# Kernel optimization log

Hardware: AMD Instinct MI355X
Metric: run time of the kernel (lower is better)

Reference implementation:

```python
import jax, jax.numpy as jnp
import numpy as np

TEMP = 0.1
QUEUE_SIZE = 512
CUTOFF_KM = 25.0
EARTH_R_KM = 6371.0088


def _normalize(x, eps=1e-12):
    # F.normalize: x / max(||x||, eps)
    n = jnp.linalg.norm(x, axis=-1, keepdims=True)
    return x / jnp.maximum(n, eps)


def _haversine_km(g1, g2):
    # g1: (B,2) [lat,lon] degrees; g2: (S,2) -> (B,S) great-circle km
    r = jnp.pi / 180.0
    lat1 = g1[:, 0:1] * r
    lon1 = g1[:, 1:2] * r
    lat2 = g2[None, :, 0] * r
    lon2 = g2[None, :, 1] * r
    dlat = lat2 - lat1
    dlon = lon2 - lon1
    a = jnp.sin(dlat / 2) ** 2 + jnp.cos(lat1) * jnp.cos(lat2) * jnp.sin(dlon / 2) ** 2
    return 2.0 * EARTH_R_KM * jnp.arcsin(jnp.sqrt(jnp.clip(a, 0.0, 1.0)))


def setup_inputs() -> dict:
    key = jax.random.key(0)
    k = jax.random.split(key, 7)
    n_aug, B, D, S = 4, 256, 768, 65536
    V = jax.random.normal(k[0], (n_aug, B, D), jnp.float32)
    L = jax.random.normal(k[1], (B, D), jnp.float32)
    gps = jnp.concatenate([
        jax.random.uniform(k[2], (B, 1), jnp.float32, -90.0, 90.0),
        jax.random.uniform(k[3], (B, 1), jnp.float32, -180.0, 180.0)], axis=1)
    support_features = jax.random.normal(k[4], (S, D), jnp.float32)
    support_gps = jnp.concatenate([
        jax.random.uniform(k[5], (S, 1), jnp.float32, -90.0, 90.0),
        jax.random.uniform(k[6], (S, 1), jnp.float32, -180.0, 180.0)], axis=1)
    return {"V": V, "L": L, "gps": gps,
            "support_features": support_features, "support_gps": support_gps}


def reference(V, L, gps, support_features, support_gps):
    # org joint embedding always from V[0]; nearest neighbour over raw support feats
    org = _normalize(V[0] * L)                                   # (B,D)
    sim = org @ support_features.T                               # (B,S)
    nn_idx = jnp.argmax(sim, axis=1)                             # (B,)
    nn = _normalize(support_features[nn_idx])                    # (B,D)

    # augmented joints for j = 1..n_aug-1
    augs = _normalize(V[1:] * L[None])                           # (J,B,D)
    # numerator always uses V[1] (as in the original code), constant over j
    num = jnp.einsum('bd,bd->b', nn, augs[0]) / TEMP             # (B,)

    # in-batch denominator: sum_i exp(nn_b . aug_{j,i} / T)
    batch_den = jnp.exp(jnp.einsum('bd,jid->jbi', nn, augs) / TEMP).sum(axis=2)  # (J,B)

    # GPS-filtered negative queue: first QUEUE_SIZE support entries > 25 km away,
    # zero-padded (zero rows contribute exp(0) = 1, matching the torch code)
    mask = _haversine_km(gps, support_gps) > CUTOFF_KM           # (B,S)
    order = jnp.argsort(jnp.where(mask, 0, 1), axis=1)[:, :QUEUE_SIZE]  # stable: kept in original order
    valid = jnp.take_along_axis(mask, order, axis=1)             # (B,Q)
    qfeat = support_features[order] * valid[..., None]           # (B,Q,D)
    queue_den = jnp.exp(jnp.einsum('bd,bqd->bq', nn, qfeat) / TEMP).sum(axis=1)  # (B,)

    den = jnp.log(batch_den + queue_den[None, :])                # (J,B)
    loss = -(num[None, :] - den).sum() / V.shape[1]
    return loss
```

## Files before the change

kernel.cpp:

```cpp
#include <hip/hip_runtime.h>
#include <hip/hip_bf16.h>

#define B_ROWS 256
#define S_SUP  65536
#define D_DIM  768
#define QSZ    512
#define NCH    12
#define ABYTES 32768
#define BBYTES 16384

typedef short bf16x8 __attribute__((ext_vector_type(8)));
typedef float f32x4  __attribute__((ext_vector_type(4)));
typedef float f32x16 __attribute__((ext_vector_type(16)));

__device__ __forceinline__ bf16x8 cvt8(float4 a, float4 b) {
  bf16x8 r;
  r[0] = (short)(__float_as_uint(a.x) >> 16);
  r[1] = (short)(__float_as_uint(a.y) >> 16);
  r[2] = (short)(__float_as_uint(a.z) >> 16);
  r[3] = (short)(__float_as_uint(a.w) >> 16);
  r[4] = (short)(__float_as_uint(b.x) >> 16);
  r[5] = (short)(__float_as_uint(b.y) >> 16);
  r[6] = (short)(__float_as_uint(b.z) >> 16);
  r[7] = (short)(__float_as_uint(b.w) >> 16);
  return r;
}

__device__ __forceinline__ void gl_lds16(const void* g, void* l) {
  __builtin_amdgcn_global_load_lds(
      (const __attribute__((address_space(1))) unsigned int*)g,
      (__attribute__((address_space(3))) unsigned int*)l, 16, 0, 0);
}

__device__ __forceinline__ float block_sum(float v) {
  __shared__ float tmp[4];
  #pragma unroll
  for (int m = 32; m >= 1; m >>= 1) v += __shfl_xor(v, m, 64);
  __syncthreads();
  if ((threadIdx.x & 63) == 0) tmp[threadIdx.x >> 6] = v;
  __syncthreads();
  return tmp[0] + tmp[1] + tmp[2] + tmp[3];
}

__device__ __forceinline__ double block_sum_d(double v) {
  __shared__ double tmp[4];
  #pragma unroll
  for (int m = 32; m >= 1; m >>= 1) v += __shfl_xor(v, m, 64);
  __syncthreads();
  if ((threadIdx.x & 63) == 0) tmp[threadIdx.x >> 6] = v;
  __syncthreads();
  return tmp[0] + tmp[1] + tmp[2] + tmp[3];
}

__global__ __launch_bounds__(256) void init_kernel(unsigned long long* gmax, double* bden) {
  int t = threadIdx.x;
  gmax[t] = 0ull;
  for (int i = t; i < 3 * B_ROWS; i += 256) bden[i] = 0.0;
}

__global__ __launch_bounds__(256) void prep_kernel(const float* __restrict__ V,
                                                   const float* __restrict__ L,
                                                   unsigned short* __restrict__ orgb,
                                                   float* __restrict__ augs) {
  int jb = blockIdx.x;
  int j = jb >> 8, b = jb & 255;
  int tid = threadIdx.x;
  __shared__ float srow[D_DIM];
  const float* v = V + ((size_t)j * B_ROWS + b) * D_DIM;
  const float* l = L + (size_t)b * D_DIM;
  float p[3]; float ssq = 0.f;
  #pragma unroll
  for (int i = 0; i < 3; ++i) {
    int k = tid + 256 * i;
    p[i] = v[k] * l[k];
    ssq += p[i] * p[i];
  }
  ssq = block_sum(ssq);
  float inv = 1.0f / fmaxf(sqrtf(ssq), 1e-12f);
  if (j == 0) {
    #pragma unroll
    for (int i = 0; i < 3; ++i) srow[tid + 256 * i] = p[i] * inv;
    __syncthreads();
    if (tid < 96) {
      int k0 = tid * 8;
      float4 f0 = *(const float4*)&srow[k0];
      float4 f1 = *(const float4*)&srow[k0 + 4];
      bf16x8 hv = cvt8(f0, f1);
      int c = k0 >> 6, g = (k0 >> 3) & 7;
      *(bf16x8*)(orgb + c * 16384 + g * 2048 + b * 8) = hv;
    }
  } else {
    float* dst = augs + ((size_t)(j - 1) * B_ROWS + b) * D_DIM;
    #pragma unroll
    for (int i = 0; i < 3; ++i) dst[tid + 256 * i] = p[i] * inv;
  }
}

__global__ __launch_bounds__(512, 4) void sim_argmax_kernel(const unsigned short* __restrict__ orgb,
                                                            const float* __restrict__ sf,
                                                            unsigned long long* __restrict__ gmax) {
  const int tid = threadIdx.x;
  const int w   = tid >> 6;
  const int l   = tid & 63;
  const int h   = l >> 5;
  const int c31 = l & 31;
  const int wr  = w >> 1;
  const int wc  = w & 1;
  const int s0  = blockIdx.x * 128;

  __shared__ __align__(16) char smem[ABYTES + BBYTES];

  f32x16 acc[4];
  #pragma unroll
  for (int t = 0; t < 4; ++t)
    #pragma unroll
    for (int r = 0; r < 16; ++r) acc[t][r] = 0.f;

  const int bs = tid >> 2;
  const int ko = (tid & 3) * 16;
  const float* bsrc0 = sf + (size_t)(s0 + bs) * D_DIM + ko;
  const int g0 = ko >> 3;
  char* bw0 = smem + ABYTES + g0 * 2048 + ((bs ^ g0) & 127) * 16;
  char* bw1 = smem + ABYTES + (g0 + 1) * 2048 + ((bs ^ (g0 + 1)) & 127) * 16;

  const char* agbase = (const char*)orgb + w * 1024 + l * 16;
  char* aldst0 = smem + 0 * 8192 + w * 1024;
  char* aldst1 = smem + 1 * 8192 + w * 1024;
  char* aldst2 = smem + 2 * 8192 + w * 1024;
  char* aldst3 = smem + 3 * 8192 + w * 1024;

  const int ar0 = wr * 64 + c31;
  const int ar1 = ar0 + 32;
  const int bs0 = wc * 64 + c31;
  const int bs1 = bs0 + 32;

  for (int c = 0; c < NCH; ++c) {
    const float4* bp = (const float4*)(bsrc0 + c * 64);
    float4 f0 = bp[0], f1 = bp[1], f2 = bp[2], f3 = bp[3];
    {
      const char* g = agbase + c * ABYTES;
      gl_lds16(g,         aldst0);
      gl_lds16(g +  8192, aldst1);
      gl_lds16(g + 16384, aldst2);
      gl_lds16(g + 24576, aldst3);
    }
    *(bf16x8*)bw0 = cvt8(f0, f1);
    *(bf16x8*)bw1 = cvt8(f2, f3);
    __syncthreads();

    #pragma unroll
    for (int ks = 0; ks < 4; ++ks) {
      int g = ks * 2 + h;
      bf16x8 a0 = *(const bf16x8*)(smem + g * 4096 + ar0 * 16);
      bf16x8 a1 = *(const bf16x8*)(smem + g * 4096 + ar1 * 16);
      bf16x8 b0 = *(const bf16x8*)(smem + ABYTES + g * 2048 + ((bs0 ^ g) & 127) * 16);
      bf16x8 b1 = *(const bf16x8*)(smem + ABYTES + g * 2048 + ((bs1 ^ g) & 127) * 16);
      acc[0] = __builtin_amdgcn_mfma_f32_32x32x16_bf16(a0, b0, acc[0], 0, 0, 0);
      acc[1] = __builtin_amdgcn_mfma_f32_32x32x16_bf16(a0, b1, acc[1], 0, 0, 0);
      acc[2] = __builtin_amdgcn_mfma_f32_32x32x16_bf16(a1, b0, acc[2], 0, 0, 0);
      acc[3] = __builtin_amdgcn_mfma_f32_32x32x16_bf16(a1, b1, acc[3], 0, 0, 0);
    }
    __syncthreads();
  }

  float* smax = (float*)smem;
  int*   sidx = (int*)(smem + 2048);
  #pragma unroll
  for (int t = 0; t < 2; ++t) {
    #pragma unroll
    for (int rg = 0; rg < 16; ++rg) {
      float v0 = acc[t * 2 + 0][rg];
      float v1 = acc[t * 2 + 1][rg];
      int i0 = s0 + wc * 64 + c31;
      int i1 = i0 + 32;
      float v; int idx;
      if (v1 > v0) { v = v1; idx = i1; } else { v = v0; idx = i0; }
      #pragma unroll
      for (int m = 1; m < 32; m <<= 1) {
        float ov = __shfl_xor(v, m, 64);
        int   oi = __shfl_xor(idx, m, 64);
        if (ov > v || (ov == v && oi < idx)) { v = ov; idx = oi; }
      }
      if (c31 == 0) {
        int row = wr * 64 + t * 32 + (rg & 3) + 8 * (rg >> 2) + 4 * h;
        smax[wc * 256 + row] = v;
        sidx[wc * 256 + row] = idx;
      }
    }
  }
  __syncthreads();
  if (tid < 256) {
    int b = tid;
    float v  = smax[b];       int idx = sidx[b];
    float ov = smax[256 + b]; int oi  = sidx[256 + b];
    if (ov > v || (ov == v && oi < idx)) { v = ov; idx = oi; }
    unsigned u = __float_as_uint(v);
    unsigned key = (u & 0x80000000u) ? ~u : (u | 0x80000000u);
    unsigned long long packed = ((unsigned long long)key << 32) |
                                (unsigned long long)(0xFFFFFFFFu - (unsigned)idx);
    if (packed > gmax[b]) atomicMax(gmax + b, packed);
  }
}

__global__ __launch_bounds__(256) void nn_kernel(const unsigned long long* __restrict__ gmax,
                                                 const float* __restrict__ sf,
                                                 const float* __restrict__ augs,
                                                 float* __restrict__ nn,
                                                 float* __restrict__ nnT,
                                                 float* __restrict__ num) {
  int b = blockIdx.x, tid = threadIdx.x;
  int idx = (int)(0xFFFFFFFFu - (unsigned)(gmax[b] & 0xFFFFFFFFull));
  const float* row = sf + (size_t)idx * D_DIM;
  float p[3]; float ssq = 0.f;
  #pragma unroll
  for (int i = 0; i < 3; ++i) { p[i] = row[tid + 256 * i]; ssq += p[i] * p[i]; }
  ssq = block_sum(ssq);
  float inv = 1.0f / fmaxf(sqrtf(ssq), 1e-12f);
  const float* a0 = augs + (size_t)b * D_DIM;
  float dot = 0.f;
  #pragma unroll
  for (int i = 0; i < 3; ++i) {
    int k = tid + 256 * i;
    float nv = p[i] * inv;
    nn[(size_t)b * D_DIM + k] = nv;
    nnT[(size_t)k * B_ROWS + b] = nv;
    dot += nv * a0[k];
  }
  dot = block_sum(dot);
  if (tid == 0) num[b] = dot * 10.0f;
}

__global__ __launch_bounds__(256) void bden_kernel(const float* __restrict__ augs,
                                                   const float* __restrict__ nnT,
                                                   double* __restrict__ bden) {
  int jc = blockIdx.x;
  int j = jc >> 6, c = jc & 63;
  int i0 = c * 4;
  __shared__ float s_aug[4 * D_DIM];
  const float* src = augs + ((size_t)j * B_ROWS + i0) * D_DIM;
  for (int idx = threadIdx.x; idx < 4 * D_DIM; idx += 256) s_aug[idx] = src[idx];
  __syncthreads();
  int b = threadIdx.x;
  float a0 = 0.f, a1 = 0.f, a2 = 0.f, a3 = 0.f;
  for (int k = 0; k < D_DIM; ++k) {
    float nv = nnT[(size_t)k * B_ROWS + b];
    a0 += nv * s_aug[k];
    a1 += nv * s_aug[D_DIM + k];
    a2 += nv * s_aug[2 * D_DIM + k];
    a3 += nv * s_aug[3 * D_DIM + k];
  }
  double v = exp((double)a0 * 10.0) + exp((double)a1 * 10.0) +
             exp((double)a2 * 10.0) + exp((double)a3 * 10.0);
  atomicAdd(&bden[j * B_ROWS + b], v);
}

__global__ __launch_bounds__(256) void queue_kernel(const float* __restrict__ gps,
                                                    const float* __restrict__ sgps,
                                                    const float* __restrict__ sf,
                                                    const float* __restrict__ nn,
                                                    double* __restrict__ qden) {
  int b = blockIdx.x, tid = threadIdx.x;
  int w = tid >> 6, lane = tid & 63;
  __shared__ int qidx[QSZ];
  __shared__ int s_count;
  __shared__ int s_wcnt[4];
  __shared__ __align__(16) float s_nn[D_DIM];
  __shared__ double s_gsum[16];
  for (int k = tid; k < D_DIM; k += 256) s_nn[k] = nn[(size_t)b * D_DIM + k];
  if (tid == 0) s_count = 0;
  __syncthreads();

  const float r = 0.017453292519943295f;
  float lat1 = gps[b * 2 + 0] * r, lon1 = gps[b * 2 + 1] * r;
  float cl1 = cosf(lat1);
  int base = 0;
  while (true) {
    int count = s_count;
    if (count >= QSZ || base >= S_SUP) break;
    int s = base + tid;
    float lat2 = sgps[s * 2 + 0] * r, lon2 = sgps[s * 2 + 1] * r;
    float sdlat = sinf((lat2 - lat1) * 0.5f);
    float sdlon = sinf((lon2 - lon1) * 0.5f);
    float a = sdlat * sdlat + cl1 * cosf(lat2) * sdlon * sdlon;
    a = fminf(fmaxf(a, 0.f), 1.f);
    float d = 2.0f * 6371.0088f * asinf(sqrtf(a));
    bool valid = d > 25.0f;

    unsigned long long m = __ballot(valid);
    int wcnt = __popcll(m);
    if (lane == 0) s_wcnt[w] = wcnt;
    __syncthreads();
    int wbase = count;
    for (int i = 0; i < w; ++i) wbase += s_wcnt[i];
    int pos = wbase + __popcll(m & ((1ull << lane) - 1ull));
    if (valid && pos < QSZ) qidx[pos] = s;
    __syncthreads();
    if (tid == 0) {
      int total = s_wcnt[0] + s_wcnt[1] + s_wcnt[2] + s_wcnt[3];
      s_count = min(QSZ, count + total);
    }
    base += 256;
    __syncthreads();
  }
  int count = s_count;

  int g  = lane >> 4;
  int l2 = lane & 15;
  double acc = 0.0;
  const float4* nn4 = (const float4*)s_nn;
  for (int q = w * 4 + g; q < count; q += 16) {
    const float4* row = (const float4*)(sf + (size_t)qidx[q] * D_DIM);
    float dot = 0.f;
    #pragma unroll
    for (int i = 0; i < 12; ++i) {
      float4 a = row[l2 + 16 * i];
      float4 nv = nn4[l2 + 16 * i];
      dot += a.x * nv.x + a.y * nv.y + a.z * nv.z + a.w * nv.w;
    }
    #pragma unroll
    for (int m2 = 8; m2 >= 1; m2 >>= 1) dot += __shfl_xor(dot, m2, 16);
    if (l2 == 0) acc += exp((double)dot * 10.0);
  }
  if (l2 == 0) s_gsum[w * 4 + g] = acc;
  __syncthreads();
  if (tid == 0) {
    double t = (double)(QSZ - count);
    #pragma unroll
    for (int i = 0; i < 16; ++i) t += s_gsum[i];
    qden[b] = t;
  }
}

__global__ __launch_bounds__(256) void loss_kernel(const float* __restrict__ num,
                                                   const double* __restrict__ bden,
                                                   const double* __restrict__ qden,
                                                   float* __restrict__ out) {
  int b = threadIdx.x;
  double q = qden[b];
  double n = (double)num[b];
  double t = 0.0;
  #pragma unroll
  for (int j = 0; j < 3; ++j) t += n - log(bden[j * B_ROWS + b] + q);
  t = block_sum_d(t);
  if (b == 0) out[0] = (float)(-t / 256.0);
}

extern "C" void kernel_launch(void* const* d_in, const int* in_sizes, int n_in,
                              void* d_out, int out_size, void* d_ws, size_t ws_size,
                              hipStream_t stream) {
  const float* V    = (const float*)d_in[0];
  const float* L    = (const float*)d_in[1];
  const float* gps  = (const float*)d_in[2];
  const float* sf   = (const float*)d_in[3];
  const float* sgps = (const float*)d_in[4];
  float* out = (float*)d_out;

  char* ws = (char*)d_ws;
  size_t off = 0;
  unsigned short* orgb = (unsigned short*)(ws + off); off += 393216;
  float* augs = (float*)(ws + off); off += 2359296;
  float* nn   = (float*)(ws + off); off += 786432;
  float* nnT  = (float*)(ws + off); off += 786432;
  float* num  = (float*)(ws + off); off += 1024;
  double* bden = (double*)(ws + off); off += 6144;
  double* qden = (double*)(ws + off); off += 2048;
  unsigned long long* gmax = (unsigned long long*)(ws + off); off += 2048;

  init_kernel<<<1, 256, 0, stream>>>(gmax, bden);
  prep_kernel<<<1024, 256, 0, stream>>>(V, L, orgb, augs);
  sim_argmax_kernel<<<S_SUP / 128, 512, 0, stream>>>(orgb, sf, gmax);
  nn_kernel<<<B_ROWS, 256, 0, stream>>>(gmax, sf, augs, nn, nnT, num);
  bden_kernel<<<192, 256, 0, stream>>>(augs, nnT, bden);
  queue_kernel<<<B_ROWS, 256, 0, stream>>>(gps, sgps, sf, nn, qden);
  loss_kernel<<<1, 256, 0, stream>>>(num, bden, qden, out);
}
```

Measured before the change: 394.4 us.

## Restructure sim GEMM: per-wave support rows direct from global, larger A chunks

The similarity/argmax kernel now has each wave own 32 support rows, loading and converting them straight from global memory into MFMA B operands with register prefetch, instead of staging them through LDS. A 256-column K-chunk of the bf16 query matrix (128 KB) goes into LDS, giving 3 chunk iterations instead of 12. Each block covers 256 support rows and reduces the argmax across 8 waves. This cuts LDS traffic for B and the number of barriers, but uses more accumulator registers and more LDS, which lowers occupancy to 2 blocks per CU and exposes direct global loads to latency.

```diff
diff --git a/kernel.cpp b/kernel.cpp
--- a/kernel.cpp
+++ b/kernel.cpp
@@ -5,9 +5,9 @@
 #define S_SUP  65536
 #define D_DIM  768
 #define QSZ    512
-#define NCH    12
-#define ABYTES 32768
-#define BBYTES 16384
+#define NCH    3
+#define CHUNK_K 256
+#define ACH_BYTES 131072
 
 typedef short bf16x8 __attribute__((ext_vector_type(8)));
 typedef float f32x4  __attribute__((ext_vector_type(4)));
@@ -86,8 +86,8 @@
       float4 f0 = *(const float4*)&srow[k0];
       float4 f1 = *(const float4*)&srow[k0 + 4];
       bf16x8 hv = cvt8(f0, f1);
-      int c = k0 >> 6, g = (k0 >> 3) & 7;
-      *(bf16x8*)(orgb + c * 16384 + g * 2048 + b * 8) = hv;
+      int c = k0 >> 8, g = (k0 >> 3) & 31;
+      *(bf16x8*)(orgb + c * 65536 + g * 2048 + b * 8) = hv;
     }
   } else {
     float* dst = augs + ((size_t)(j - 1) * B_ROWS + b) * D_DIM;
@@ -96,7 +96,7 @@
   }
 }
 
-__global__ __launch_bounds__(512, 4) void sim_argmax_kernel(const unsigned short* __restrict__ orgb,
+__global__ __launch_bounds__(512, 2) void sim_argmax_kernel(const unsigned short* __restrict__ orgb,
                                                             const float* __restrict__ sf,
                                                             unsigned long long* __restrict__ gmax) {
   const int tid = threadIdx.x;
@@ -104,77 +104,59 @@
   const int l   = tid & 63;
   const int h   = l >> 5;
   const int c31 = l & 31;
-  const int wr  = w >> 1;
-  const int wc  = w & 1;
-  const int s0  = blockIdx.x * 128;
-
-  __shared__ __align__(16) char smem[ABYTES + BBYTES];
-
-  f32x16 acc[4];
-  #pragma unroll
-  for (int t = 0; t < 4; ++t)
-    #pragma unroll
-    for (int r = 0; r < 16; ++r) acc[t][r] = 0.f;
-
-  const int bs = tid >> 2;
-  const int ko = (tid & 3) * 16;
-  const float* bsrc0 = sf + (size_t)(s0 + bs) * D_DIM + ko;
-  const int g0 = ko >> 3;
-  char* bw0 = smem + ABYTES + g0 * 2048 + ((bs ^ g0) & 127) * 16;
-  char* bw1 = smem + ABYTES + (g0 + 1) * 2048 + ((bs ^ (g0 + 1)) & 127) * 16;
-
-  const char* agbase = (const char*)orgb + w * 1024 + l * 16;
-  char* aldst0 = smem + 0 * 8192 + w * 1024;
-  char* aldst1 = smem + 1 * 8192 + w * 1024;
-  char* aldst2 = smem + 2 * 8192 + w * 1024;
-  char* aldst3 = smem + 3 * 8192 + w * 1024;
-
-  const int ar0 = wr * 64 + c31;
-  const int ar1 = ar0 + 32;
-  const int bs0 = wc * 64 + c31;
-  const int bs1 = bs0 + 32;
+  const int s0  = blockIdx.x * 256;
+  const int myrow = s0 + w * 32 + c31;
+
+  __shared__ __align__(16) char smem[ACH_BYTES];
+
+  f32x16 accs[8];
+  #pragma unroll
+  for (int t = 0; t < 8; ++t)
+    #pragma unroll
+    for (int r = 0; r < 16; ++r) accs[t][r] = 0.f;
+
+  const char* sfb = (const char*)sf + (size_t)myrow * 3072 + h * 32;
+  const char* agbase = (const char*)orgb + tid * 16;
+  char* adst = smem + tid * 16;
 
   for (int c = 0; c < NCH; ++c) {
-    const float4* bp = (const float4*)(bsrc0 + c * 64);
-    float4 f0 = bp[0], f1 = bp[1], f2 = bp[2], f3 = bp[3];
     {
-      const char* g = agbase + c * ABYTES;
-      gl_lds16(g,         aldst0);
-      gl_lds16(g +  8192, aldst1);
-      gl_lds16(g + 16384, aldst2);
-      gl_lds16(g + 24576, aldst3);
-    }
-    *(bf16x8*)bw0 = cvt8(f0, f1);
-    *(bf16x8*)bw1 = cvt8(f2, f3);
-    __syncthreads();
-
-    #pragma unroll
-    for (int ks = 0; ks < 4; ++ks) {
-      int g = ks * 2 + h;
-      bf16x8 a0 = *(const bf16x8*)(smem + g * 4096 + ar0 * 16);
-      bf16x8 a1 = *(const bf16x8*)(smem + g * 4096 + ar1 * 16);
-      bf16x8 b0 = *(const bf16x8*)(smem + ABYTES + g * 2048 + ((bs0 ^ g) & 127) * 16);
-      bf16x8 b1 = *(const bf16x8*)(smem + ABYTES + g * 2048 + ((bs1 ^ g) & 127) * 16);
-      acc[0] = __builtin_amdgcn_mfma_f32_32x32x16_bf16(a0, b0, acc[0], 0, 0, 0);
-      acc[1] = __builtin_amdgcn_mfma_f32_32x32x16_bf16(a0, b1, acc[1], 0, 0, 0);
-      acc[2] = __builtin_amdgcn_mfma_f32_32x32x16_bf16(a1, b0, acc[2], 0, 0, 0);
-      acc[3] = __builtin_amdgcn_mfma_f32_32x32x16_bf16(a1, b1, acc[3], 0, 0, 0);
+      const char* g = agbase + c * ACH_BYTES;
+      #pragma unroll
+      for (int i = 0; i < 16; ++i)
+        gl_lds16(g + i * 8192, adst + i * 8192);
+    }
+    __syncthreads();
+
+    const char* brow = sfb + c * 1024;
+    float4 nb0 = *(const float4*)(brow);
+    float4 nb1 = *(const float4*)(brow + 16);
+    #pragma unroll
+    for (int ks = 0; ks < 16; ++ks) {
+      float4 cb0 = nb0, cb1 = nb1;
+      if (ks < 15) {
+        nb0 = *(const float4*)(brow + (ks + 1) * 64);
+        nb1 = *(const float4*)(brow + (ks + 1) * 64 + 16);
+      }
+      bf16x8 bf = cvt8(cb0, cb1);
+      const char* ab = smem + (ks * 2 + h) * 4096 + c31 * 16;
+      #pragma unroll
+      for (int rt = 0; rt < 8; ++rt) {
+        bf16x8 af = *(const bf16x8*)(ab + rt * 512);
+        accs[rt] = __builtin_amdgcn_mfma_f32_32x32x16_bf16(af, bf, accs[rt], 0, 0, 0);
+      }
     }
     __syncthreads();
   }
 
   float* smax = (float*)smem;
-  int*   sidx = (int*)(smem + 2048);
-  #pragma unroll
-  for (int t = 0; t < 2; ++t) {
+  int*   sidx = (int*)(smem + 8192);
+  #pragma unroll
+  for (int rt = 0; rt < 8; ++rt) {
     #pragma unroll
     for (int rg = 0; rg < 16; ++rg) {
-      float v0 = acc[t * 2 + 0][rg];
-      float v1 = acc[t * 2 + 1][rg];
-      int i0 = s0 + wc * 64 + c31;
-      int i1 = i0 + 32;
-      float v; int idx;
-      if (v1 > v0) { v = v1; idx = i1; } else { v = v0; idx = i0; }
+      float v = accs[rt][rg];
+      int idx = myrow;
       #pragma unroll
       for (int m = 1; m < 32; m <<= 1) {
         float ov = __shfl_xor(v, m, 64);
@@ -182,23 +164,26 @@
         if (ov > v || (ov == v && oi < idx)) { v = ov; idx = oi; }
       }
       if (c31 == 0) {
-        int row = wr * 64 + t * 32 + (rg & 3) + 8 * (rg >> 2) + 4 * h;
-        smax[wc * 256 + row] = v;
-        sidx[wc * 256 + row] = idx;
+        int row = rt * 32 + (rg & 3) + 8 * (rg >> 2) + 4 * h;
+        smax[w * 256 + row] = v;
+        sidx[w * 256 + row] = idx;
       }
     }
   }
   __syncthreads();
   if (tid < 256) {
-    int b = tid;
-    float v  = smax[b];       int idx = sidx[b];
-    float ov = smax[256 + b]; int oi  = sidx[256 + b];
-    if (ov > v || (ov == v && oi < idx)) { v = ov; idx = oi; }
+    int row = tid;
+    float v = smax[row]; int idx = sidx[row];
+    #pragma unroll
+    for (int w2 = 1; w2 < 8; ++w2) {
+      float ov = smax[w2 * 256 + row]; int oi = sidx[w2 * 256 + row];
+      if (ov > v || (ov == v && oi < idx)) { v = ov; idx = oi; }
+    }
     unsigned u = __float_as_uint(v);
     unsigned key = (u & 0x80000000u) ? ~u : (u | 0x80000000u);
     unsigned long long packed = ((unsigned long long)key << 32) |
                                 (unsigned long long)(0xFFFFFFFFu - (unsigned)idx);
-    if (packed > gmax[b]) atomicMax(gmax + b, packed);
+    if (packed > gmax[row]) atomicMax(gmax + row, packed);
   }
 }
 
@@ -368,7 +353,7 @@
 
   init_kernel<<<1, 256, 0, stream>>>(gmax, bden);
   prep_kernel<<<1024, 256, 0, stream>>>(V, L, orgb, augs);
-  sim_argmax_kernel<<<S_SUP / 128, 512, 0, stream>>>(orgb, sf, gmax);
+  sim_argmax_kernel<<<S_SUP / 256, 512, 0, stream>>>(orgb, sf, gmax);
   nn_kernel<<<B_ROWS, 256, 0, stream>>>(gmax, sf, augs, nn, nnT, num);
   bden_kernel<<<192, 256, 0, stream>>>(augs, nnT, bden);
   queue_kernel<<<B_ROWS, 256, 0, stream>>>(gps, sgps, sf, nn, qden);
```

New measurement: 440.8 us. +11.8%, slower.

## Double-buffer LDS tiles in sim-argmax GEMM with register prefetch

Applied to the files above, without the earlier changes.

Restructures the main similarity-argmax GEMM loop so that global loads for the next K-tile go into registers while MFMAs run on the current LDS buffer, then get stored into the alternate buffer. This uses one barrier per iteration instead of two and drops the global_load_lds direct path. LDS grows to 96 KB and launch bounds fall from 4 to 2 blocks per CU, which reduces occupancy and latency hiding across blocks.

```diff
diff --git a/kernel.cpp b/kernel.cpp
--- a/kernel.cpp
+++ b/kernel.cpp
@@ -5,9 +5,10 @@
 #define S_SUP  65536
 #define D_DIM  768
 #define QSZ    512
-#define NCH    12
-#define ABYTES 32768
-#define BBYTES 16384
+#define NKT    12
+#define ASTEP  32768
+#define BSTEP  16384
+#define BBASE  65536
 
 typedef short bf16x8 __attribute__((ext_vector_type(8)));
 typedef float f32x4  __attribute__((ext_vector_type(4)));
@@ -26,12 +27,6 @@
   return r;
 }
 
-__device__ __forceinline__ void gl_lds16(const void* g, void* l) {
-  __builtin_amdgcn_global_load_lds(
-      (const __attribute__((address_space(1))) unsigned int*)g,
-      (__attribute__((address_space(3))) unsigned int*)l, 16, 0, 0);
-}
-
 __device__ __forceinline__ float block_sum(float v) {
   __shared__ float tmp[4];
   #pragma unroll
@@ -96,7 +91,7 @@
   }
 }
 
-__global__ __launch_bounds__(512, 4) void sim_argmax_kernel(const unsigned short* __restrict__ orgb,
+__global__ __launch_bounds__(512, 2) void sim_argmax_kernel(const unsigned short* __restrict__ orgb,
                                                             const float* __restrict__ sf,
                                                             unsigned long long* __restrict__ gmax) {
   const int tid = threadIdx.x;
@@ -108,7 +103,7 @@
   const int wc  = w & 1;
   const int s0  = blockIdx.x * 128;
 
-  __shared__ __align__(16) char smem[ABYTES + BBYTES];
+  __shared__ __align__(16) char smem[98304];
 
   f32x16 acc[4];
   #pragma unroll
@@ -116,62 +111,94 @@
     #pragma unroll
     for (int r = 0; r < 16; ++r) acc[t][r] = 0.f;
 
-  const int bs = tid >> 2;
-  const int ko = (tid & 3) * 16;
-  const float* bsrc0 = sf + (size_t)(s0 + bs) * D_DIM + ko;
-  const int g0 = ko >> 3;
-  char* bw0 = smem + ABYTES + g0 * 2048 + ((bs ^ g0) & 127) * 16;
-  char* bw1 = smem + ABYTES + (g0 + 1) * 2048 + ((bs ^ (g0 + 1)) & 127) * 16;
-
-  const char* agbase = (const char*)orgb + w * 1024 + l * 16;
-  char* aldst0 = smem + 0 * 8192 + w * 1024;
-  char* aldst1 = smem + 1 * 8192 + w * 1024;
-  char* aldst2 = smem + 2 * 8192 + w * 1024;
-  char* aldst3 = smem + 3 * 8192 + w * 1024;
-
-  const int ar0 = wr * 64 + c31;
-  const int ar1 = ar0 + 32;
-  const int bs0 = wc * 64 + c31;
-  const int bs1 = bs0 + 32;
-
-  for (int c = 0; c < NCH; ++c) {
-    const float4* bp = (const float4*)(bsrc0 + c * 64);
-    float4 f0 = bp[0], f1 = bp[1], f2 = bp[2], f3 = bp[3];
-    {
-      const char* g = agbase + c * ABYTES;
-      gl_lds16(g,         aldst0);
-      gl_lds16(g +  8192, aldst1);
-      gl_lds16(g + 16384, aldst2);
-      gl_lds16(g + 24576, aldst3);
-    }
-    *(bf16x8*)bw0 = cvt8(f0, f1);
-    *(bf16x8*)bw1 = cvt8(f2, f3);
-    __syncthreads();
-
+  const char* agbase = (const char*)orgb + tid * 16;
+  const int bsr = tid >> 2;
+  const int bq  = tid & 3;
+  const float* bgbase = sf + (size_t)(s0 + bsr) * D_DIM + bq * 16;
+  const int bg0 = bq * 2;
+  char* bdst0 = smem + BBASE + bg0 * 2048 + (((bsr ^ bg0) & 127) << 4);
+  char* bdst1 = smem + BBASE + (bg0 + 1) * 2048 + (((bsr ^ (bg0 + 1)) & 127) << 4);
+
+  const int arow0 = (wr * 64 + c31) * 16;
+  const int bcol0 = wc * 64 + c31;
+
+  bf16x8 av0, av1, av2, av3;
+  float4 f0, f1, f2, f3;
+
+  {
+    const char* ag = agbase;
+    av0 = *(const bf16x8*)(ag);
+    av1 = *(const bf16x8*)(ag + 8192);
+    av2 = *(const bf16x8*)(ag + 16384);
+    av3 = *(const bf16x8*)(ag + 24576);
+    const float4* bp = (const float4*)bgbase;
+    f0 = bp[0]; f1 = bp[1]; f2 = bp[2]; f3 = bp[3];
+    char* ad = smem + tid * 16;
+    *(bf16x8*)(ad)         = av0;
+    *(bf16x8*)(ad + 8192)  = av1;
+    *(bf16x8*)(ad + 16384) = av2;
+    *(bf16x8*)(ad + 24576) = av3;
+    *(bf16x8*)bdst0 = cvt8(f0, f1);
+    *(bf16x8*)bdst1 = cvt8(f2, f3);
+  }
+  asm volatile("s_waitcnt lgkmcnt(0)" ::: "memory");
+  __builtin_amdgcn_s_barrier();
+  __builtin_amdgcn_sched_barrier(0);
+
+  for (int kt = 0; kt < NKT; ++kt) {
+    const int cur = kt & 1;
+    if (kt < NKT - 1) {
+      const char* ag = agbase + (kt + 1) * ASTEP;
+      av0 = *(const bf16x8*)(ag);
+      av1 = *(const bf16x8*)(ag + 8192);
+      av2 = *(const bf16x8*)(ag + 16384);
+      av3 = *(const bf16x8*)(ag + 24576);
+      const float4* bp = (const float4*)(bgbase + (size_t)(kt + 1) * 64);
+      f0 = bp[0]; f1 = bp[1]; f2 = bp[2]; f3 = bp[3];
+    }
+    __builtin_amdgcn_sched_barrier(0);
+
+    const char* abuf = smem + cur * ASTEP;
+    const char* bbuf = smem + BBASE + cur * BSTEP;
     #pragma unroll
     for (int ks = 0; ks < 4; ++ks) {
-      int g = ks * 2 + h;
-      bf16x8 a0 = *(const bf16x8*)(smem + g * 4096 + ar0 * 16);
-      bf16x8 a1 = *(const bf16x8*)(smem + g * 4096 + ar1 * 16);
-      bf16x8 b0 = *(const bf16x8*)(smem + ABYTES + g * 2048 + ((bs0 ^ g) & 127) * 16);
-      bf16x8 b1 = *(const bf16x8*)(smem + ABYTES + g * 2048 + ((bs1 ^ g) & 127) * 16);
+      const int g = ks * 2 + h;
+      bf16x8 a0 = *(const bf16x8*)(abuf + g * 4096 + arow0);
+      bf16x8 a1 = *(const bf16x8*)(abuf + g * 4096 + arow0 + 512);
+      bf16x8 b0 = *(const bf16x8*)(bbuf + g * 2048 + (((bcol0      ) ^ g) & 127) * 16);
+      bf16x8 b1 = *(const bf16x8*)(bbuf + g * 2048 + (((bcol0 + 32 ) ^ g) & 127) * 16);
       acc[0] = __builtin_amdgcn_mfma_f32_32x32x16_bf16(a0, b0, acc[0], 0, 0, 0);
       acc[1] = __builtin_amdgcn_mfma_f32_32x32x16_bf16(a0, b1, acc[1], 0, 0, 0);
       acc[2] = __builtin_amdgcn_mfma_f32_32x32x16_bf16(a1, b0, acc[2], 0, 0, 0);
       acc[3] = __builtin_amdgcn_mfma_f32_32x32x16_bf16(a1, b1, acc[3], 0, 0, 0);
     }
-    __syncthreads();
+    __builtin_amdgcn_sched_barrier(0);
+
+    if (kt < NKT - 1) {
+      const int nxt = cur ^ 1;
+      char* ad = smem + nxt * ASTEP + tid * 16;
+      *(bf16x8*)(ad)         = av0;
+      *(bf16x8*)(ad + 8192)  = av1;
+      *(bf16x8*)(ad + 16384) = av2;
+      *(bf16x8*)(ad + 24576) = av3;
+      char* bd = smem + nxt * BSTEP;
+      *(bf16x8*)(bd + (bdst0 - smem)) = cvt8(f0, f1);
+      *(bf16x8*)(bd + (bdst1 - smem)) = cvt8(f2, f3);
+      asm volatile("s_waitcnt lgkmcnt(0)" ::: "memory");
+      __builtin_amdgcn_s_barrier();
+      __builtin_amdgcn_sched_barrier(0);
+    }
   }
 
   float* smax = (float*)smem;
   int*   sidx = (int*)(smem + 2048);
   #pragma unroll
-  for (int t = 0; t < 2; ++t) {
+  for (int rt = 0; rt < 2; ++rt) {
     #pragma unroll
     for (int rg = 0; rg < 16; ++rg) {
-      float v0 = acc[t * 2 + 0][rg];
-      float v1 = acc[t * 2 + 1][rg];
-      int i0 = s0 + wc * 64 + c31;
+      float v0 = acc[rt * 2 + 0][rg];
+      float v1 = acc[rt * 2 + 1][rg];
+      int i0 = s0 + bcol0;
       int i1 = i0 + 32;
       float v; int idx;
       if (v1 > v0) { v = v1; idx = i1; } else { v = v0; idx = i0; }
@@ -182,7 +209,7 @@
         if (ov > v || (ov == v && oi < idx)) { v = ov; idx = oi; }
       }
       if (c31 == 0) {
-        int row = wr * 64 + t * 32 + (rg & 3) + 8 * (rg >> 2) + 4 * h;
+        int row = wr * 64 + rt * 32 + (rg & 3) + 8 * (rg >> 2) + 4 * h;
         smax[wc * 256 + row] = v;
         sidx[wc * 256 + row] = idx;
       }
```

Result: slower. 405.4 us (+2.8%).

## Split sim-argmax blocks into two row halves with smaller K chunks

Applied to the files above, without the earlier changes.

Retiles the similarity/argmax GEMM so each 256-thread block handles 128 query rows × 128 support columns, with K chunks of 32 and a new A panel layout from prep_kernel. This cuts shared memory per block from 48 KB to 16 KB and doubles the block count, aiming for higher occupancy and better latency hiding. In exchange, every support-feature tile is read from global memory and converted to bf16 twice (once per row half), increasing traffic on the large fp32 support matrix. It also doubles the number of barriers per unit of work.

```diff
diff --git a/kernel.cpp b/kernel.cpp
--- a/kernel.cpp
+++ b/kernel.cpp
@@ -5,9 +5,9 @@
 #define S_SUP  65536
 #define D_DIM  768
 #define QSZ    512
-#define NCH    12
-#define ABYTES 32768
-#define BBYTES 16384
+#define NCH    24
+#define ACH    8192
+#define APANEL 196608
 
 typedef short bf16x8 __attribute__((ext_vector_type(8)));
 typedef float f32x4  __attribute__((ext_vector_type(4)));
@@ -86,8 +86,9 @@
       float4 f0 = *(const float4*)&srow[k0];
       float4 f1 = *(const float4*)&srow[k0 + 4];
       bf16x8 hv = cvt8(f0, f1);
-      int c = k0 >> 6, g = (k0 >> 3) & 7;
-      *(bf16x8*)(orgb + c * 16384 + g * 2048 + b * 8) = hv;
+      int rp = b >> 7, r = b & 127;
+      int c = k0 >> 5, g = (k0 >> 3) & 3;
+      *(bf16x8*)(orgb + ((((size_t)rp * 24 + c) * 4 + g) * 128 + r) * 8) = hv;
     }
   } else {
     float* dst = augs + ((size_t)(j - 1) * B_ROWS + b) * D_DIM;
@@ -96,7 +97,7 @@
   }
 }
 
-__global__ __launch_bounds__(512, 4) void sim_argmax_kernel(const unsigned short* __restrict__ orgb,
+__global__ __launch_bounds__(256, 4) void sim_argmax_kernel(const unsigned short* __restrict__ orgb,
                                                             const float* __restrict__ sf,
                                                             unsigned long long* __restrict__ gmax) {
   const int tid = threadIdx.x;
@@ -104,11 +105,13 @@
   const int l   = tid & 63;
   const int h   = l >> 5;
   const int c31 = l & 31;
-  const int wr  = w >> 1;
-  const int wc  = w & 1;
-  const int s0  = blockIdx.x * 128;
-
-  __shared__ __align__(16) char smem[ABYTES + BBYTES];
+  const int wr  = w & 1;
+  const int wc  = w >> 1;
+  const int rp  = blockIdx.x & 1;
+  const int cp  = blockIdx.x >> 1;
+  const int s0  = cp * 128;
+
+  __shared__ __align__(16) char smem[16384];
 
   f32x16 acc[4];
   #pragma unroll
@@ -116,45 +119,41 @@
     #pragma unroll
     for (int r = 0; r < 16; ++r) acc[t][r] = 0.f;
 
-  const int bs = tid >> 2;
-  const int ko = (tid & 3) * 16;
-  const float* bsrc0 = sf + (size_t)(s0 + bs) * D_DIM + ko;
-  const int g0 = ko >> 3;
-  char* bw0 = smem + ABYTES + g0 * 2048 + ((bs ^ g0) & 127) * 16;
-  char* bw1 = smem + ABYTES + (g0 + 1) * 2048 + ((bs ^ (g0 + 1)) & 127) * 16;
-
-  const char* agbase = (const char*)orgb + w * 1024 + l * 16;
-  char* aldst0 = smem + 0 * 8192 + w * 1024;
-  char* aldst1 = smem + 1 * 8192 + w * 1024;
-  char* aldst2 = smem + 2 * 8192 + w * 1024;
-  char* aldst3 = smem + 3 * 8192 + w * 1024;
-
-  const int ar0 = wr * 64 + c31;
-  const int ar1 = ar0 + 32;
-  const int bs0 = wc * 64 + c31;
-  const int bs1 = bs0 + 32;
+  const char* agb = (const char*)orgb + (size_t)rp * APANEL + tid * 16;
+  char* adst = smem + tid * 16;
+
+  const int bcol = tid >> 1;
+  const int kh   = tid & 1;
+  const float* bsrc = sf + (size_t)(s0 + bcol) * D_DIM + kh * 16;
+  const int g0 = kh * 2;
+  char* bw0 = smem + 8192 + g0 * 2048 + (((bcol ^ g0) & 127) << 4);
+  char* bw1 = smem + 8192 + (g0 + 1) * 2048 + (((bcol ^ (g0 + 1)) & 127) << 4);
+
+  const int arow = (wr * 64 + c31) * 16;
+  const int bc0  = wc * 64 + c31;
+  const int bc1  = bc0 + 32;
 
   for (int c = 0; c < NCH; ++c) {
-    const float4* bp = (const float4*)(bsrc0 + c * 64);
-    float4 f0 = bp[0], f1 = bp[1], f2 = bp[2], f3 = bp[3];
     {
-      const char* g = agbase + c * ABYTES;
-      gl_lds16(g,         aldst0);
-      gl_lds16(g +  8192, aldst1);
-      gl_lds16(g + 16384, aldst2);
-      gl_lds16(g + 24576, aldst3);
-    }
-    *(bf16x8*)bw0 = cvt8(f0, f1);
-    *(bf16x8*)bw1 = cvt8(f2, f3);
-    __syncthreads();
-
-    #pragma unroll
-    for (int ks = 0; ks < 4; ++ks) {
-      int g = ks * 2 + h;
-      bf16x8 a0 = *(const bf16x8*)(smem + g * 4096 + ar0 * 16);
-      bf16x8 a1 = *(const bf16x8*)(smem + g * 4096 + ar1 * 16);
-      bf16x8 b0 = *(const bf16x8*)(smem + ABYTES + g * 2048 + ((bs0 ^ g) & 127) * 16);
-      bf16x8 b1 = *(const bf16x8*)(smem + ABYTES + g * 2048 + ((bs1 ^ g) & 127) * 16);
+      const char* g = agb + c * ACH;
+      gl_lds16(g,        adst);
+      gl_lds16(g + 4096, adst + 4096);
+    }
+    {
+      const float4* bp = (const float4*)(bsrc + c * 32);
+      float4 f0 = bp[0], f1 = bp[1], f2 = bp[2], f3 = bp[3];
+      *(bf16x8*)bw0 = cvt8(f0, f1);
+      *(bf16x8*)bw1 = cvt8(f2, f3);
+    }
+    __syncthreads();
+
+    #pragma unroll
+    for (int ks = 0; ks < 2; ++ks) {
+      const int g = ks * 2 + h;
+      bf16x8 a0 = *(const bf16x8*)(smem + g * 2048 + arow);
+      bf16x8 a1 = *(const bf16x8*)(smem + g * 2048 + arow + 512);
+      bf16x8 b0 = *(const bf16x8*)(smem + 8192 + g * 2048 + (((bc0 ^ g) & 127) << 4));
+      bf16x8 b1 = *(const bf16x8*)(smem + 8192 + g * 2048 + (((bc1 ^ g) & 127) << 4));
       acc[0] = __builtin_amdgcn_mfma_f32_32x32x16_bf16(a0, b0, acc[0], 0, 0, 0);
       acc[1] = __builtin_amdgcn_mfma_f32_32x32x16_bf16(a0, b1, acc[1], 0, 0, 0);
       acc[2] = __builtin_amdgcn_mfma_f32_32x32x16_bf16(a1, b0, acc[2], 0, 0, 0);
@@ -166,13 +165,13 @@
   float* smax = (float*)smem;
   int*   sidx = (int*)(smem + 2048);
   #pragma unroll
-  for (int t = 0; t < 2; ++t) {
+  for (int rt = 0; rt < 2; ++rt) {
     #pragma unroll
     for (int rg = 0; rg < 16; ++rg) {
-      float v0 = acc[t * 2 + 0][rg];
-      float v1 = acc[t * 2 + 1][rg];
-      int i0 = s0 + wc * 64 + c31;
-      int i1 = i0 + 32;
+      float v0 = acc[rt * 2 + 0][rg];
+      float v1 = acc[rt * 2 + 1][rg];
+      int i0 = s0 + bc0;
+      int i1 = s0 + bc1;
       float v; int idx;
       if (v1 > v0) { v = v1; idx = i1; } else { v = v0; idx = i0; }
       #pragma unroll
@@ -182,22 +181,23 @@
         if (ov > v || (ov == v && oi < idx)) { v = ov; idx = oi; }
       }
       if (c31 == 0) {
-        int row = wr * 64 + t * 32 + (rg & 3) + 8 * (rg >> 2) + 4 * h;
-        smax[wc * 256 + row] = v;
-        sidx[wc * 256 + row] = idx;
+        int row = wr * 64 + rt * 32 + (rg & 3) + 8 * (rg >> 2) + 4 * h;
+        smax[wc * 128 + row] = v;
+        sidx[wc * 128 + row] = idx;
       }
     }
   }
   __syncthreads();
-  if (tid < 256) {
-    int b = tid;
-    float v  = smax[b];       int idx = sidx[b];
-    float ov = smax[256 + b]; int oi  = sidx[256 + b];
+  if (tid < 128) {
+    int row = tid;
+    float v  = smax[row];       int idx = sidx[row];
+    float ov = smax[128 + row]; int oi  = sidx[128 + row];
     if (ov > v || (ov == v && oi < idx)) { v = ov; idx = oi; }
     unsigned u = __float_as_uint(v);
     unsigned key = (u & 0x80000000u) ? ~u : (u | 0x80000000u);
     unsigned long long packed = ((unsigned long long)key << 32) |
                                 (unsigned long long)(0xFFFFFFFFu - (unsigned)idx);
+    int b = rp * 128 + row;
     if (packed > gmax[b]) atomicMax(gmax + b, packed);
   }
 }
@@ -368,7 +368,7 @@
 
   init_kernel<<<1, 256, 0, stream>>>(gmax, bden);
   prep_kernel<<<1024, 256, 0, stream>>>(V, L, orgb, augs);
-  sim_argmax_kernel<<<S_SUP / 128, 512, 0, stream>>>(orgb, sf, gmax);
+  sim_argmax_kernel<<<(S_SUP / 128) * 2, 256, 0, stream>>>(orgb, sf, gmax);
   nn_kernel<<<B_ROWS, 256, 0, stream>>>(gmax, sf, augs, nn, nnT, num);
   bden_kernel<<<192, 256, 0, stream>>>(augs, nnT, bden);
   queue_kernel<<<B_ROWS, 256, 0, stream>>>(gps, sgps, sf, nn, qden);
```

Measured after the change: 408.7 us. +3.6%, slower.
